# Kernel optimization log

Measured on AMD Instinct MI355X. Metric: run time of the kernel, lower is better.

Reference implementation:

```python
import jax, jax.numpy as jnp
import numpy as np

B, T, D_MODEL, HEAD_SIZE = 8, 1024, 1024, 64
BLOCK_SIZE = 1024  # == max_relative_pos


def setup_inputs() -> dict:
    key = jax.random.key(0)
    ks = jax.random.split(key, 7)
    s = 1.0 / np.sqrt(D_MODEL)
    return {
        "x": jax.random.normal(ks[0], (B, T, D_MODEL), dtype=jnp.float32),
        "Wk": jax.random.normal(ks[1], (D_MODEL, HEAD_SIZE), dtype=jnp.float32) * s,
        "bk": jax.random.normal(ks[2], (HEAD_SIZE,), dtype=jnp.float32) * 0.02,
        "Wq": jax.random.normal(ks[3], (D_MODEL, HEAD_SIZE), dtype=jnp.float32) * s,
        "bq": jax.random.normal(ks[4], (HEAD_SIZE,), dtype=jnp.float32) * 0.02,
        "Wv": jax.random.normal(ks[5], (D_MODEL, HEAD_SIZE), dtype=jnp.float32) * s,
        "rel_emb": jax.random.normal(ks[6], (2 * BLOCK_SIZE + 1, HEAD_SIZE), dtype=jnp.float32) * 0.02,
        "mask": 1,
    }


def reference(x, Wk, bk, Wq, bq, Wv, rel_emb, mask):
    Bb, Tt, _ = x.shape
    hs = Wk.shape[1]
    max_rel = (rel_emb.shape[0] - 1) // 2

    k = x @ Wk + bk          # [B,T,hs]
    q = x @ Wq + bq          # [B,T,hs]
    v = x @ Wv               # [B,T,hs]

    pos = jnp.arange(Tt)
    idx = jnp.clip(pos[:, None] - pos[None, :], -max_rel, max_rel) + max_rel
    r = rel_emb[idx]         # [T,T,hs], r[i,j] = emb(clip(i-j))

    # scores[b,i,j] = (q[b,i] + r[i,j]) . (k[b,j] + r[j,i]) / sqrt(hs)
    scale = 1.0 / np.sqrt(hs).astype(np.float32)
    scores = (
        jnp.einsum("bid,bjd->bij", q, k)
        + jnp.einsum("bid,jid->bij", q, r)   # q_i . r[j,i]
        + jnp.einsum("ijd,bjd->bij", r, k)   # r[i,j] . k_j
        + jnp.einsum("ijd,jid->ij", r, r)[None]  # r[i,j] . r[j,i]
    ) * scale

    if mask:  # static Python int -> causal mask, matches tril masked_fill
        causal = jnp.tril(jnp.ones((Tt, Tt), dtype=bool))
        scores = jnp.where(causal, scores, jnp.float32(-jnp.inf))

    w = jax.nn.softmax(scores, axis=-1)  # dropout is identity in eval mode
    return w @ v  # [B,T,hs]
```

## Files before the change

kernel.cpp:

```cpp
#include <hip/hip_runtime.h>
#include <hip/hip_bf16.h>
#include <math.h>


typedef __hip_bfloat16 bf16;
typedef __attribute__((ext_vector_type(8))) short short8;
typedef __attribute__((ext_vector_type(4))) float f32x4;

#define NTILE32 528
#define MFMA16(a, b, c) __builtin_amdgcn_mfma_f32_16x16x32_bf16(a, b, c, 0, 0, 0)

__device__ __forceinline__ float bf2f(bf16 h) { return __bfloat162float(h); }
__device__ __forceinline__ bf16 f2bf(float f) { return __float2bfloat16(f); }
__device__ __forceinline__ short bfs(float f) {
  bf16 h = __float2bfloat16(f);
  return *(short*)&h;
}

union U16 {
  uint4 u;
  short8 s;
};
__device__ __forceinline__ short8 ldfrag(const bf16* p) {
  U16 x;
  x.u = *(const uint4*)p;
  return x.s;
}

__global__ __launch_bounds__(256) void prep_kernel(
    const float* __restrict__ Wk, const float* __restrict__ Wq, const float* __restrict__ Wv,
    const float* __restrict__ E, bf16* __restrict__ WT, bf16* __restrict__ Ep,
    bf16* __restrict__ Erev, float* __restrict__ rrG, float* __restrict__ zeroBase) {
  const int bid = blockIdx.x, t = threadIdx.x;
  if (bid < 768) {
    int idx = bid * 256 + t;
    int sel = idx >> 16, r = idx & 65535;
    int n = r >> 10, kk = r & 1023;
    const float* W = (sel == 0) ? Wk : (sel == 1) ? Wq : Wv;
    WT[idx] = f2bf(W[kk * 64 + n]);
  } else if (bid < 1281) {
    int idx = (bid - 768) * 256 + t;
    if (idx < 2049 * 64) {
      int tt = idx >> 6, d = idx & 63;
      Ep[idx] = f2bf(E[idx]);
      Erev[idx] = f2bf(E[(size_t)(2048 - tt) * 64 + d]);
    }
  } else if (bid < 1537) {
    int dlt = ((bid - 1281) << 2) + (t >> 6);
    int d = t & 63;
    float p = E[(size_t)(1024 + dlt) * 64 + d] * E[(size_t)(1024 - dlt) * 64 + d];
#pragma unroll
    for (int off = 32; off > 0; off >>= 1) p += __shfl_down(p, off);
    if (d == 0) rrG[64 + dlt] = p;
  } else {
    int idx4 = (bid - 1537) * 256 + t;
    if (idx4 < 2048)
      *(float4*)(zeroBase + idx4 * 4) = make_float4(0.f, 0.f, 0.f, 0.f);
  }
}

__global__ __launch_bounds__(256, 2) void qkv_mfma(
    const float* __restrict__ x, const bf16* __restrict__ WT,
    const float* __restrict__ bk, const float* __restrict__ bq,
    bf16* __restrict__ qB, bf16* __restrict__ kB, bf16* __restrict__ vT) {
  const int R0 = blockIdx.x << 4;
  const int t = threadIdx.x;
  const int lane = t & 63, wave = t >> 6;
  const int m = lane & 15, quad = lane >> 4;

  __shared__ float RED[4][16][196];
  __shared__ bf16 VTS[64][24];

  const float* xrow = x + (size_t)(R0 + m) * 1024 + (wave << 8);
  f32x4 acc[3][4];
#pragma unroll
  for (int s = 0; s < 3; ++s)
#pragma unroll
    for (int c = 0; c < 4; ++c) acc[s][c] = (f32x4){0.f, 0.f, 0.f, 0.f};

#pragma unroll
  for (int ks = 0; ks < 8; ++ks) {
    const int k0 = ks * 32 + quad * 8;
    float4 xa = *(const float4*)(xrow + k0);
    float4 xb = *(const float4*)(xrow + k0 + 4);
    short8 a;
    a[0] = bfs(xa.x); a[1] = bfs(xa.y); a[2] = bfs(xa.z); a[3] = bfs(xa.w);
    a[4] = bfs(xb.x); a[5] = bfs(xb.y); a[6] = bfs(xb.z); a[7] = bfs(xb.w);
    const int kg = (wave << 8) + k0;
#pragma unroll
    for (int sel = 0; sel < 3; ++sel)
#pragma unroll
      for (int ct = 0; ct < 4; ++ct) {
        const bf16* bb = WT + ((size_t)(sel * 64 + ct * 16 + m) << 10) + kg;
        acc[sel][ct] = MFMA16(a, ldfrag(bb), acc[sel][ct]);
      }
  }

#pragma unroll
  for (int sel = 0; sel < 3; ++sel)
#pragma unroll
    for (int ct = 0; ct < 4; ++ct)
#pragma unroll
      for (int r = 0; r < 4; ++r)
        RED[wave][quad * 4 + r][sel * 64 + ct * 16 + m] = acc[sel][ct][r];
  __syncthreads();

#pragma unroll
  for (int e = 0; e < 12; ++e) {
    int idx = e * 256 + t;
    int row = idx / 192, c = idx - row * 192;
    float s = RED[0][row][c] + RED[1][row][c] + RED[2][row][c] + RED[3][row][c];
    int sel = c >> 6, col = c & 63;
    size_t grow = (size_t)(R0 + row);
    if (sel == 0) kB[grow * 64 + col] = f2bf(s + bk[col]);
    else if (sel == 1) qB[grow * 64 + col] = f2bf(s + bq[col]);
    else VTS[col][row] = f2bf(s);
  }
  __syncthreads();
  {
    int dd = t >> 2, h = (t & 3) << 2;
    int b = R0 >> 10, tloc = R0 & 1023;
    *(uint2*)(vT + ((size_t)((b << 6) + dd) << 10) + tloc + h) = *(const uint2*)&VTS[dd][h];
  }
}

__global__ __launch_bounds__(256, 4) void flash_mfma(
    const bf16* __restrict__ qB, const bf16* __restrict__ kB, const bf16* __restrict__ vT,
    const bf16* __restrict__ Ep, const bf16* __restrict__ Erev, const float* __restrict__ rrG,
    float* __restrict__ Opart, float* __restrict__ Lacc) {
  const int t = threadIdx.x;
  const int lane = t & 63, wave = t >> 6;
  const int m = lane & 15, quad = lane >> 4;

  const int g = (blockIdx.x << 2) + wave;
  const int b = g / NTILE32;
  const int r0 = g - b * NTILE32;
  int it = (int)((sqrtf(8.f * r0 + 1.f) - 1.f) * 0.5f);
  while ((it + 1) * (it + 2) / 2 <= r0) ++it;
  while (it * (it + 1) / 2 > r0) --it;
  const int jt = r0 - it * (it + 1) / 2;
  const int I0 = it << 5, J0 = jt << 5;
  const int D = I0 - J0, w0 = D - 32;

  __shared__ __align__(16) bf16 M2S[4][32][68];
  __shared__ __align__(16) bf16 M3S[4][32][68];
  bf16 (*M2)[68] = M2S[wave];
  bf16 (*M3)[68] = M3S[wave];
  bf16 (*PS)[40] = (bf16(*)[40]) & M3S[wave][0][0];

  const bf16* qb = qB + ((size_t)((b << 10) + I0) << 6);
  const bf16* kb = kB + ((size_t)((b << 10) + J0) << 6);
  short8 aq[2][2], kf[2][2];
#pragma unroll
  for (int rt = 0; rt < 2; ++rt)
#pragma unroll
    for (int ks = 0; ks < 2; ++ks) {
      aq[rt][ks] = ldfrag(qb + ((rt * 16 + m) << 6) + ks * 32 + quad * 8);
      kf[rt][ks] = ldfrag(kb + ((rt * 16 + m) << 6) + ks * 32 + quad * 8);
    }

  const bf16* erb = Erev + ((size_t)(1024 + w0) << 6);
  const bf16* epb = Ep + ((size_t)(1024 + w0) << 6);
#pragma unroll
  for (int ct = 0; ct < 4; ++ct) {
    const bf16* b2p = erb + ((size_t)(ct * 16 + m) << 6) + quad * 8;
    const bf16* b3p = epb + ((size_t)(ct * 16 + m) << 6) + quad * 8;
    const short8 b20 = ldfrag(b2p);
    const short8 b21 = ldfrag(b2p + 32);
    const short8 b30 = ldfrag(b3p);
    const short8 b31 = ldfrag(b3p + 32);
    const float rv = rrG[64 + w0 + ct * 16 + m];
#pragma unroll
    for (int rt = 0; rt < 2; ++rt) {
      f32x4 c2 = (f32x4){0.f, 0.f, 0.f, 0.f};
      c2 = MFMA16(aq[rt][0], b20, c2);
      c2 = MFMA16(aq[rt][1], b21, c2);
      f32x4 c3 = (f32x4){0.f, 0.f, 0.f, 0.f};
      c3 = MFMA16(kf[rt][0], b30, c3);
      c3 = MFMA16(kf[rt][1], b31, c3);
#pragma unroll
      for (int r = 0; r < 4; ++r) {
        M2[rt * 16 + quad * 4 + r][ct * 16 + m] = f2bf(c2[r] + rv);
        M3[rt * 16 + quad * 4 + r][ct * 16 + m] = f2bf(c3[r]);
      }
    }
  }

  f32x4 acc[2][2];
#pragma unroll
  for (int rt = 0; rt < 2; ++rt)
#pragma unroll
    for (int ct = 0; ct < 2; ++ct) {
      f32x4 c = (f32x4){0.f, 0.f, 0.f, 0.f};
      c = MFMA16(aq[rt][0], kf[ct][0], c);
      c = MFMA16(aq[rt][1], kf[ct][1], c);
      acc[rt][ct] = c;
    }

  float sc[2][2][4], lr[2][4];
#pragma unroll
  for (int rt = 0; rt < 2; ++rt)
#pragma unroll
    for (int r = 0; r < 4; ++r) lr[rt][r] = 0.f;
#pragma unroll
  for (int ct = 0; ct < 2; ++ct) {
    const int uj = ct * 16 + m;
#pragma unroll
    for (int rt = 0; rt < 2; ++rt)
#pragma unroll
      for (int r = 0; r < 4; ++r) {
        const int ui = rt * 16 + quad * 4 + r;
        float p = 0.f;
        if (ui - uj + D >= 0) {
          const int wi = ui - uj + 32;
          const float sv = (acc[rt][ct][r] + bf2f(M2[ui][wi]) + bf2f(M3[uj][wi])) * 0.125f;
          p = __expf(sv - 8.0f);
        }
        sc[ct][rt][r] = p;
        lr[rt][r] += p;
      }
  }
#pragma unroll
  for (int rt = 0; rt < 2; ++rt)
#pragma unroll
    for (int r = 0; r < 4; ++r) {
#pragma unroll
      for (int off = 1; off < 16; off <<= 1) lr[rt][r] += __shfl_xor(lr[rt][r], off);
    }
  if (m == 0) {
#pragma unroll
    for (int rt = 0; rt < 2; ++rt)
#pragma unroll
      for (int r = 0; r < 4; ++r)
        atomicAdd(&Lacc[(b << 10) + I0 + rt * 16 + quad * 4 + r], lr[rt][r]);
  }

#pragma unroll
  for (int ct = 0; ct < 2; ++ct)
#pragma unroll
    for (int rt = 0; rt < 2; ++rt)
#pragma unroll
      for (int r = 0; r < 4; ++r)
        PS[rt * 16 + quad * 4 + r][ct * 16 + m] = f2bf(sc[ct][rt][r]);

  short8 ap[2];
#pragma unroll
  for (int rt = 0; rt < 2; ++rt) ap[rt] = ldfrag(&PS[rt * 16 + m][quad * 8]);
  float* obp = Opart + ((size_t)(b * NTILE32 + r0) << 11);
#pragma unroll
  for (int ct = 0; ct < 4; ++ct) {
    const short8 vf = ldfrag(vT + ((size_t)(b * 64 + ct * 16 + m) << 10) + J0 + quad * 8);
#pragma unroll
    for (int rt = 0; rt < 2; ++rt) {
      f32x4 o = (f32x4){0.f, 0.f, 0.f, 0.f};
      o = MFMA16(ap[rt], vf, o);
#pragma unroll
      for (int r = 0; r < 4; ++r)
        obp[(size_t)((rt * 16 + quad * 4 + r) * 64 + ct * 16 + m)] = o[r];
    }
  }
}

__global__ __launch_bounds__(256) void normalize_kernel(
    const float* __restrict__ Opart, const float* __restrict__ Lacc, float* __restrict__ out) {
  const int idx = blockIdx.x * 256 + threadIdx.x;
  const int b = idx >> 16;
  const int rem = idx & 65535;
  const int i = rem >> 6, d = rem & 63;
  const int it = i >> 5;
  const int base = (it * (it + 1)) >> 1;
  const float* sp = Opart + ((size_t)(b * NTILE32 + base) << 11) + ((i & 31) << 6) + d;
  float s0 = 0.f, s1 = 0.f;
  int jt = 0;
  for (; jt + 1 <= it; jt += 2) {
    s0 += sp[(size_t)jt << 11];
    s1 += sp[(size_t)(jt + 1) << 11];
  }
  if (jt <= it) s0 += sp[(size_t)jt << 11];
  out[idx] = (s0 + s1) / Lacc[idx >> 6];
}

extern "C" void kernel_launch(void* const* d_in, const int* in_sizes, int n_in,
                              void* d_out, int out_size, void* d_ws, size_t ws_size,
                              hipStream_t stream) {
  const float* x = (const float*)d_in[0];
  const float* Wk = (const float*)d_in[1];
  const float* bk = (const float*)d_in[2];
  const float* Wq = (const float*)d_in[3];
  const float* bq = (const float*)d_in[4];
  const float* Wv = (const float*)d_in[5];
  const float* E = (const float*)d_in[6];
  float* out = (float*)d_out;

  float* wsf = (float*)d_ws;
  float* Opart = wsf;
  float* Lacc = wsf + 8650752;
  float* rrG = Lacc + 8192;
  bf16* qB = (bf16*)(rrG + 1152);
  bf16* kB = qB + 524288;
  bf16* vT = kB + 524288;
  bf16* Ep = vT + 524288;
  bf16* Erev = Ep + 131200;
  bf16* WT = Erev + 131200;

  prep_kernel<<<1545, 256, 0, stream>>>(Wk, Wq, Wv, E, WT, Ep, Erev, rrG, Lacc);
  qkv_mfma<<<512, 256, 0, stream>>>(x, WT, bk, bq, qB, kB, vT);
  flash_mfma<<<1056, 256, 0, stream>>>(qB, kB, vT, Ep, Erev, rrG, Opart, Lacc);
  normalize_kernel<<<2048, 256, 0, stream>>>(Opart, Lacc, out);
}
```

Measured before the change: 144.5 us.

## Process two key tiles per wave to halve partial outputs and reuse Q

Each wave now handles up to two consecutive 32-wide key tiles for the same query tile, accumulating P·V in registers before writing a single partial. This halves the number of Opart partials written and later summed by the normalize kernel, and reuses the loaded Q fragments across both tiles. The task indexing changes from triangular to a paired scheme (272 tasks per batch), and launch bounds drop to 3 waves/SIMD to allow more registers. The cost is a longer serial chain per wave and fewer blocks in flight.

```diff
diff --git a/kernel.cpp b/kernel.cpp
--- a/kernel.cpp
+++ b/kernel.cpp
@@ -7,7 +7,7 @@
 typedef __attribute__((ext_vector_type(8))) short short8;
 typedef __attribute__((ext_vector_type(4))) float f32x4;
 
-#define NTILE32 528
+#define NTASK 272
 #define MFMA16(a, b, c) __builtin_amdgcn_mfma_f32_16x16x32_bf16(a, b, c, 0, 0, 0)
 
 __device__ __forceinline__ float bf2f(bf16 h) { return __bfloat162float(h); }
@@ -124,7 +124,7 @@
   }
 }
 
-__global__ __launch_bounds__(256, 4) void flash_mfma(
+__global__ __launch_bounds__(256, 3) void flash_mfma(
     const bf16* __restrict__ qB, const bf16* __restrict__ kB, const bf16* __restrict__ vT,
     const bf16* __restrict__ Ep, const bf16* __restrict__ Erev, const float* __restrict__ rrG,
     float* __restrict__ Opart, float* __restrict__ Lacc) {
@@ -132,15 +132,17 @@
   const int lane = t & 63, wave = t >> 6;
   const int m = lane & 15, quad = lane >> 4;
 
-  const int g = (blockIdx.x << 2) + wave;
-  const int b = g / NTILE32;
-  const int r0 = g - b * NTILE32;
-  int it = (int)((sqrtf(8.f * r0 + 1.f) - 1.f) * 0.5f);
-  while ((it + 1) * (it + 2) / 2 <= r0) ++it;
-  while (it * (it + 1) / 2 > r0) --it;
-  const int jt = r0 - it * (it + 1) / 2;
-  const int I0 = it << 5, J0 = jt << 5;
-  const int D = I0 - J0, w0 = D - 32;
+  const int gt = (blockIdx.x << 2) + wave;
+  const int b = gt / NTASK;
+  const int u = gt - b * NTASK;
+  int it = (int)(2.f * sqrtf((float)(u + 1))) - 1;
+  if (it < 0) it = 0;
+  if (it > 31) it = 31;
+  while (it < 31 && (((it + 2) * (it + 2)) >> 2) <= u) ++it;
+  while (it > 0 && (((it + 1) * (it + 1)) >> 2) > u) --it;
+  const int p = u - (((it + 1) * (it + 1)) >> 2);
+  const int I0 = it << 5;
+  const int nt = (2 * p + 1 <= it) ? 2 : 1;
 
   __shared__ __align__(16) bf16 M2S[4][32][68];
   __shared__ __align__(16) bf16 M3S[4][32][68];
@@ -149,77 +151,114 @@
   bf16 (*PS)[40] = (bf16(*)[40]) & M3S[wave][0][0];
 
   const bf16* qb = qB + ((size_t)((b << 10) + I0) << 6);
-  const bf16* kb = kB + ((size_t)((b << 10) + J0) << 6);
-  short8 aq[2][2], kf[2][2];
+  short8 aq[2][2];
 #pragma unroll
   for (int rt = 0; rt < 2; ++rt)
 #pragma unroll
-    for (int ks = 0; ks < 2; ++ks) {
+    for (int ks = 0; ks < 2; ++ks)
       aq[rt][ks] = ldfrag(qb + ((rt * 16 + m) << 6) + ks * 32 + quad * 8);
-      kf[rt][ks] = ldfrag(kb + ((rt * 16 + m) << 6) + ks * 32 + quad * 8);
-    }
-
-  const bf16* erb = Erev + ((size_t)(1024 + w0) << 6);
-  const bf16* epb = Ep + ((size_t)(1024 + w0) << 6);
-#pragma unroll
-  for (int ct = 0; ct < 4; ++ct) {
-    const bf16* b2p = erb + ((size_t)(ct * 16 + m) << 6) + quad * 8;
-    const bf16* b3p = epb + ((size_t)(ct * 16 + m) << 6) + quad * 8;
-    const short8 b20 = ldfrag(b2p);
-    const short8 b21 = ldfrag(b2p + 32);
-    const short8 b30 = ldfrag(b3p);
-    const short8 b31 = ldfrag(b3p + 32);
-    const float rv = rrG[64 + w0 + ct * 16 + m];
-#pragma unroll
-    for (int rt = 0; rt < 2; ++rt) {
-      f32x4 c2 = (f32x4){0.f, 0.f, 0.f, 0.f};
-      c2 = MFMA16(aq[rt][0], b20, c2);
-      c2 = MFMA16(aq[rt][1], b21, c2);
-      f32x4 c3 = (f32x4){0.f, 0.f, 0.f, 0.f};
-      c3 = MFMA16(kf[rt][0], b30, c3);
-      c3 = MFMA16(kf[rt][1], b31, c3);
-#pragma unroll
-      for (int r = 0; r < 4; ++r) {
-        M2[rt * 16 + quad * 4 + r][ct * 16 + m] = f2bf(c2[r] + rv);
-        M3[rt * 16 + quad * 4 + r][ct * 16 + m] = f2bf(c3[r]);
+
+  f32x4 osum[2][4];
+#pragma unroll
+  for (int rt = 0; rt < 2; ++rt)
+#pragma unroll
+    for (int ct = 0; ct < 4; ++ct) osum[rt][ct] = (f32x4){0.f, 0.f, 0.f, 0.f};
+  float lr[2][4];
+#pragma unroll
+  for (int rt = 0; rt < 2; ++rt)
+#pragma unroll
+    for (int r = 0; r < 4; ++r) lr[rt][r] = 0.f;
+
+  for (int s = 0; s < nt; ++s) {
+    const int jt = 2 * p + s;
+    const int J0 = jt << 5;
+    const int D = I0 - J0, w0 = D - 32;
+
+    const bf16* kb = kB + ((size_t)((b << 10) + J0) << 6);
+    short8 kf[2][2];
+#pragma unroll
+    for (int rt = 0; rt < 2; ++rt)
+#pragma unroll
+      for (int ks = 0; ks < 2; ++ks)
+        kf[rt][ks] = ldfrag(kb + ((rt * 16 + m) << 6) + ks * 32 + quad * 8);
+
+    const bf16* erb = Erev + ((size_t)(1024 + w0) << 6);
+    const bf16* epb = Ep + ((size_t)(1024 + w0) << 6);
+#pragma unroll
+    for (int ct = 0; ct < 4; ++ct) {
+      const bf16* b2p = erb + ((size_t)(ct * 16 + m) << 6) + quad * 8;
+      const bf16* b3p = epb + ((size_t)(ct * 16 + m) << 6) + quad * 8;
+      const short8 b20 = ldfrag(b2p);
+      const short8 b21 = ldfrag(b2p + 32);
+      const short8 b30 = ldfrag(b3p);
+      const short8 b31 = ldfrag(b3p + 32);
+      const float rv = rrG[64 + w0 + ct * 16 + m];
+#pragma unroll
+      for (int rt = 0; rt < 2; ++rt) {
+        f32x4 c2 = (f32x4){0.f, 0.f, 0.f, 0.f};
+        c2 = MFMA16(aq[rt][0], b20, c2);
+        c2 = MFMA16(aq[rt][1], b21, c2);
+        f32x4 c3 = (f32x4){0.f, 0.f, 0.f, 0.f};
+        c3 = MFMA16(kf[rt][0], b30, c3);
+        c3 = MFMA16(kf[rt][1], b31, c3);
+#pragma unroll
+        for (int r = 0; r < 4; ++r) {
+          M2[rt * 16 + quad * 4 + r][ct * 16 + m] = f2bf(c2[r] + rv);
+          M3[rt * 16 + quad * 4 + r][ct * 16 + m] = f2bf(c3[r]);
+        }
       }
     }
-  }
-
-  f32x4 acc[2][2];
-#pragma unroll
-  for (int rt = 0; rt < 2; ++rt)
+
+    f32x4 acc[2][2];
+#pragma unroll
+    for (int rt = 0; rt < 2; ++rt)
+#pragma unroll
+      for (int ct = 0; ct < 2; ++ct) {
+        f32x4 c = (f32x4){0.f, 0.f, 0.f, 0.f};
+        c = MFMA16(aq[rt][0], kf[ct][0], c);
+        c = MFMA16(aq[rt][1], kf[ct][1], c);
+        acc[rt][ct] = c;
+      }
+
+    float sc[2][2][4];
 #pragma unroll
     for (int ct = 0; ct < 2; ++ct) {
-      f32x4 c = (f32x4){0.f, 0.f, 0.f, 0.f};
-      c = MFMA16(aq[rt][0], kf[ct][0], c);
-      c = MFMA16(aq[rt][1], kf[ct][1], c);
-      acc[rt][ct] = c;
-    }
-
-  float sc[2][2][4], lr[2][4];
-#pragma unroll
-  for (int rt = 0; rt < 2; ++rt)
-#pragma unroll
-    for (int r = 0; r < 4; ++r) lr[rt][r] = 0.f;
-#pragma unroll
-  for (int ct = 0; ct < 2; ++ct) {
-    const int uj = ct * 16 + m;
-#pragma unroll
-    for (int rt = 0; rt < 2; ++rt)
-#pragma unroll
-      for (int r = 0; r < 4; ++r) {
-        const int ui = rt * 16 + quad * 4 + r;
-        float p = 0.f;
-        if (ui - uj + D >= 0) {
-          const int wi = ui - uj + 32;
-          const float sv = (acc[rt][ct][r] + bf2f(M2[ui][wi]) + bf2f(M3[uj][wi])) * 0.125f;
-          p = __expf(sv - 8.0f);
+      const int uj = ct * 16 + m;
+#pragma unroll
+      for (int rt = 0; rt < 2; ++rt)
+#pragma unroll
+        for (int r = 0; r < 4; ++r) {
+          const int ui = rt * 16 + quad * 4 + r;
+          float pv = 0.f;
+          if (ui - uj + D >= 0) {
+            const int wi = ui - uj + 32;
+            const float sv = (acc[rt][ct][r] + bf2f(M2[ui][wi]) + bf2f(M3[uj][wi])) * 0.125f;
+            pv = __expf(sv - 8.0f);
+          }
+          sc[ct][rt][r] = pv;
+          lr[rt][r] += pv;
         }
-        sc[ct][rt][r] = p;
-        lr[rt][r] += p;
-      }
-  }
+    }
+
+#pragma unroll
+    for (int ct = 0; ct < 2; ++ct)
+#pragma unroll
+      for (int rt = 0; rt < 2; ++rt)
+#pragma unroll
+        for (int r = 0; r < 4; ++r)
+          PS[rt * 16 + quad * 4 + r][ct * 16 + m] = f2bf(sc[ct][rt][r]);
+
+    short8 ap[2];
+#pragma unroll
+    for (int rt = 0; rt < 2; ++rt) ap[rt] = ldfrag(&PS[rt * 16 + m][quad * 8]);
+#pragma unroll
+    for (int ct = 0; ct < 4; ++ct) {
+      const short8 vf = ldfrag(vT + ((size_t)(b * 64 + ct * 16 + m) << 10) + J0 + quad * 8);
+#pragma unroll
+      for (int rt = 0; rt < 2; ++rt) osum[rt][ct] = MFMA16(ap[rt], vf, osum[rt][ct]);
+    }
+  }
+
 #pragma unroll
   for (int rt = 0; rt < 2; ++rt)
 #pragma unroll
@@ -234,31 +273,14 @@
       for (int r = 0; r < 4; ++r)
         atomicAdd(&Lacc[(b << 10) + I0 + rt * 16 + quad * 4 + r], lr[rt][r]);
   }
-
-#pragma unroll
-  for (int ct = 0; ct < 2; ++ct)
+  float* obp = Opart + ((size_t)(b * NTASK + u) << 11);
+#pragma unroll
+  for (int ct = 0; ct < 4; ++ct)
 #pragma unroll
     for (int rt = 0; rt < 2; ++rt)
 #pragma unroll
       for (int r = 0; r < 4; ++r)
-        PS[rt * 16 + quad * 4 + r][ct * 16 + m] = f2bf(sc[ct][rt][r]);
-
-  short8 ap[2];
-#pragma unroll
-  for (int rt = 0; rt < 2; ++rt) ap[rt] = ldfrag(&PS[rt * 16 + m][quad * 8]);
-  float* obp = Opart + ((size_t)(b * NTILE32 + r0) << 11);
-#pragma unroll
-  for (int ct = 0; ct < 4; ++ct) {
-    const short8 vf = ldfrag(vT + ((size_t)(b * 64 + ct * 16 + m) << 10) + J0 + quad * 8);
-#pragma unroll
-    for (int rt = 0; rt < 2; ++rt) {
-      f32x4 o = (f32x4){0.f, 0.f, 0.f, 0.f};
-      o = MFMA16(ap[rt], vf, o);
-#pragma unroll
-      for (int r = 0; r < 4; ++r)
-        obp[(size_t)((rt * 16 + quad * 4 + r) * 64 + ct * 16 + m)] = o[r];
-    }
-  }
+        obp[(size_t)((rt * 16 + quad * 4 + r) * 64 + ct * 16 + m)] = osum[rt][ct][r];
 }
 
 __global__ __launch_bounds__(256) void normalize_kernel(
@@ -268,15 +290,16 @@
   const int rem = idx & 65535;
   const int i = rem >> 6, d = rem & 63;
   const int it = i >> 5;
-  const int base = (it * (it + 1)) >> 1;
-  const float* sp = Opart + ((size_t)(b * NTILE32 + base) << 11) + ((i & 31) << 6) + d;
+  const int base = ((it + 1) * (it + 1)) >> 2;
+  const int nw = (it + 2) >> 1;
+  const float* sp = Opart + ((size_t)(b * NTASK + base) << 11) + ((i & 31) << 6) + d;
   float s0 = 0.f, s1 = 0.f;
-  int jt = 0;
-  for (; jt + 1 <= it; jt += 2) {
-    s0 += sp[(size_t)jt << 11];
-    s1 += sp[(size_t)(jt + 1) << 11];
-  }
-  if (jt <= it) s0 += sp[(size_t)jt << 11];
+  int w = 0;
+  for (; w + 1 < nw; w += 2) {
+    s0 += sp[(size_t)w << 11];
+    s1 += sp[(size_t)(w + 1) << 11];
+  }
+  if (w < nw) s0 += sp[(size_t)w << 11];
   out[idx] = (s0 + s1) / Lacc[idx >> 6];
 }
 
@@ -294,7 +317,7 @@
 
   float* wsf = (float*)d_ws;
   float* Opart = wsf;
-  float* Lacc = wsf + 8650752;
+  float* Lacc = wsf + 4456448;
   float* rrG = Lacc + 8192;
   bf16* qB = (bf16*)(rrG + 1152);
   bf16* kB = qB + 524288;
@@ -305,6 +328,6 @@
 
   prep_kernel<<<1545, 256, 0, stream>>>(Wk, Wq, Wv, E, WT, Ep, Erev, rrG, Lacc);
   qkv_mfma<<<512, 256, 0, stream>>>(x, WT, bk, bq, qB, kB, vT);
-  flash_mfma<<<1056, 256, 0, stream>>>(qB, kB, vT, Ep, Erev, rrG, Opart, Lacc);
+  flash_mfma<<<544, 256, 0, stream>>>(qB, kB, vT, Ep, Erev, rrG, Opart, Lacc);
   normalize_kernel<<<2048, 256, 0, stream>>>(Opart, Lacc, out);
 }
```

After: 149.2 us. +3.2%, slower.
